# Performance work log

Hardware: AMD Instinct MI355X
Metric: run time of the kernel (lower is better)

## Reference

```python
import jax, jax.numpy as jnp
import numpy as np

B, C, F, G = 256, 4096, 64, 512   # batch, candidates, features, max taxi groups per sample
H1, H2 = 128, 128                 # scorer hidden dims
HB = 32                           # taxi bias net hidden dim
NEG = -1e9


def setup_inputs() -> dict:
    key = jax.random.key(0)
    ks = jax.random.split(key, 8)
    feats = jax.random.normal(ks[0], (B, C, F), jnp.float32)
    gids = jax.random.randint(ks[1], (B, C), -1, G)            # -1 = defer
    mask = (jax.random.uniform(ks[2], (B, C)) < 0.9).astype(jnp.float32)
    x_with_meta = jnp.concatenate(
        [feats, gids.astype(jnp.float32)[..., None], mask[..., None]], axis=-1)

    def lin(k, i, o):
        return (jax.random.normal(k, (i, o), jnp.float32) / np.sqrt(i)).astype(jnp.float32)

    return {
        "x_with_meta": x_with_meta,
        "W0": lin(ks[3], F, H1),  "b0": jnp.zeros((H1,), jnp.float32),
        "W1": lin(ks[4], H1, H2), "b1": jnp.zeros((H2,), jnp.float32),
        "W2": lin(ks[5], H2, 1),  "b2": jnp.zeros((1,), jnp.float32),
        "Wb0": lin(ks[6], 3, HB), "bb0": jnp.zeros((HB,), jnp.float32),
        "Wb1": lin(ks[7], HB, 1), "bb1": jnp.zeros((1,), jnp.float32),
    }


def _forward(x_with_meta, W0, b0, W1, b1, W2, b2, Wb0, bb0, Wb1, bb1):
    mask = x_with_meta[..., -1]                     # [B, C]
    gids = x_with_meta[..., -2].astype(jnp.int32)   # [B, C], -1 = defer
    feats = x_with_meta[..., :-2]                   # [B, C, F]

    # CandidateScorerMLP (dropout is identity at inference)
    h = jax.nn.relu(feats @ W0 + b0)
    h = jax.nn.relu(h @ W1 + b1)
    raw = (h @ W2 + b2)[..., 0]                     # [B, C]
    raw = jnp.where(mask > 0.0, raw, NEG)

    valid = (mask > 0.0) & (gids >= 0)              # [B, C]
    nseg = B * G + 1                                # +1 dummy segment for invalid/defer
    seg = jnp.where(valid, jnp.arange(B, dtype=jnp.int32)[:, None] * G + gids, B * G)
    segf = seg.reshape(-1)
    validf = valid.reshape(-1)
    rawf = raw.reshape(-1)

    cnt = jax.ops.segment_sum(validf.astype(jnp.float32), segf, num_segments=nseg)
    ssum = jax.ops.segment_sum(jnp.where(validf, rawf, 0.0), segf, num_segments=nseg)
    smax = jax.ops.segment_max(jnp.where(validf, rawf, NEG), segf, num_segments=nseg)
    smax = jnp.where(cnt > 0.0, smax, 0.0)          # sanitize empty segments
    mean = ssum / jnp.maximum(cnt, 1.0)
    multi = cnt > 1.0                               # normalization only for group size > 1

    # Per-group taxi quality bias from pooled stats [max, mean, size]
    stats = jnp.where(multi[:, None], jnp.stack([smax, mean, cnt], axis=-1), 0.0)  # [nseg, 3]
    bias = (jax.nn.relu(stats @ Wb0 + bb0) @ Wb1 + bb1)[:, 0]                      # [nseg]

    mean_c = mean[segf].reshape(B, C)
    max_c = smax[segf].reshape(B, C)
    bias_c = bias[segf].reshape(B, C)
    apply = valid & multi[segf].reshape(B, C)

    # raw - mean + max - 0.5*(max - raw) + bias  ==  1.5*raw - mean + 0.5*max + bias
    fair = jnp.where(apply, 1.5 * raw - mean_c + 0.5 * max_c + bias_c, raw)
    fair = jnp.where(mask > 0.0, fair, NEG)
    return fair, mask


def reference(x_with_meta, W0, b0, W1, b1, W2, b2, Wb0, bb0, Wb1, bb1):
    return _forward(x_with_meta, W0, b0, W1, b1, W2, b2, Wb0, bb0, Wb1, bb1)
```

## Files before the change

kernel.cpp:

```cpp
#include <hip/hip_runtime.h>
#include <hip/hip_bf16.h>

#define NB   256
#define NC   4096
#define NG   512
#define NH   128
#define NELEM (NB*NC)
#define LDX  66
#define NEGV (-1000000000.0f)
#define TILES 16

typedef __attribute__((ext_vector_type(8))) short short8;
typedef __attribute__((ext_vector_type(4))) float f32x4;

__device__ __forceinline__ unsigned pack2(float x, float y) {
    return (__float_as_uint(y) & 0xFFFF0000u) | (__float_as_uint(x) >> 16);
}
__device__ __forceinline__ unsigned short f2bf(float f) {
    unsigned u = __float_as_uint(f);
    return (unsigned short)((u + 0x7FFFu + ((u >> 16) & 1u)) >> 16);
}
__device__ __forceinline__ unsigned encf(float f) {
    unsigned u = __float_as_uint(f);
    return (u & 0x80000000u) ? ~u : (u | 0x80000000u);
}
__device__ __forceinline__ float decf(unsigned u) {
    unsigned v = (u & 0x80000000u) ? (u ^ 0x80000000u) : ~u;
    return __uint_as_float(v);
}
__device__ __forceinline__ f32x4 mfma_bf16(short8 a, short8 b, f32x4 c) {
    return __builtin_amdgcn_mfma_f32_16x16x32_bf16(a, b, c, 0, 0, 0);
}
__device__ __forceinline__ f32x4 mfma_fp8(long a, long b, f32x4 c) {
    return __builtin_amdgcn_mfma_f32_16x16x32_fp8_fp8(a, b, c, 0, 0, 0);
}

__device__ __forceinline__ void gload16(const float* g, float* lds) {
    __builtin_amdgcn_global_load_lds(
        (const __attribute__((address_space(1))) void*)g,
        (__attribute__((address_space(3))) void*)lds,
        16, 0, 0);
}

__global__ __launch_bounds__(512, 2) void k_fused(
        const float* __restrict__ X,
        const float* __restrict__ W0, const float* __restrict__ W1,
        const float* __restrict__ b0, const float* __restrict__ b1,
        const float* __restrict__ W2, const float* __restrict__ b2p,
        const float* __restrict__ Wb0, const float* __restrict__ bb0,
        const float* __restrict__ Wb1, const float* __restrict__ bb1,
        float* __restrict__ out) {
    __shared__ __align__(16) unsigned char sW1f[16384];
    __shared__ __align__(16) float sFeat[8][2048];
    __shared__ __align__(16) unsigned char sHs[8][4096];
    __shared__ float sB0[128];
    __shared__ float sB1W2[256];
    __shared__ __align__(16) float sraw[4096];
    __shared__ unsigned short smc[4096];
    __shared__ unsigned scnt[512];
    __shared__ float    ssum[512];
    __shared__ unsigned smx[512];
    __shared__ float    sdelta[512];
    __shared__ unsigned char smulti[512];

    const int t = threadIdx.x, w = t >> 6, l = t & 63;
    const int l15 = l & 15, g = l >> 4;
    const int rx = l15 & 7;
    const int b = blockIdx.x;

    float* fw = sFeat[w];
    unsigned char* hs = sHs[w];
    const size_t rowwave0 = (size_t)b * NC + w * 32;
    const int lrow0 = w * 32;

    const int r4 = l >> 4, sl = l & 15;
    const int offE = r4 * LDX + ((sl ^ r4) << 2);
    const int offO = r4 * LDX + ((sl ^ (r4 + 4)) << 2);

    {
        const float* gb = X + rowwave0 * LDX;
#pragma unroll
        for (int k = 0; k < 8; ++k)
            gload16(gb + k * 4 * LDX + ((k & 1) ? offO : offE), fw + k * 256);
    }
    float2 mt = make_float2(0.f, 0.f), mtN = make_float2(0.f, 0.f);
    if (l < 32) mt = *(const float2*)(X + (rowwave0 + l) * LDX + 64);

    unsigned short* sW0s = (unsigned short*)sraw;
    {
        const int j = t & 127, kq = t >> 7;
        unsigned pk[8];
#pragma unroll
        for (int kk = 0; kk < 16; kk += 2) {
            float v0 = W0[(kq * 16 + kk)     * NH + j];
            float v1 = W0[(kq * 16 + kk + 1) * NH + j];
            pk[kk >> 1] = (unsigned)f2bf(v0) | ((unsigned)f2bf(v1) << 16);
        }
        unsigned short* dst = sW0s + j * 64 + kq * 16;
        ((uint4*)dst)[0] = make_uint4(pk[0], pk[1], pk[2], pk[3]);
        ((uint4*)dst)[1] = make_uint4(pk[4], pk[5], pk[6], pk[7]);
    }
#pragma unroll
    for (int it = 0; it < 4; ++it) {
        const int j = t & 127, u = (t >> 7) + it * 4;
        float v[8];
#pragma unroll
        for (int d = 0; d < 8; ++d) v[d] = W1[(u * 8 + d) * NH + j];
        unsigned lo = (unsigned)__builtin_amdgcn_cvt_pk_fp8_f32(v[0], v[1], 0, false);
        lo = (unsigned)__builtin_amdgcn_cvt_pk_fp8_f32(v[2], v[3], (int)lo, true);
        unsigned hi = (unsigned)__builtin_amdgcn_cvt_pk_fp8_f32(v[4], v[5], 0, false);
        hi = (unsigned)__builtin_amdgcn_cvt_pk_fp8_f32(v[6], v[7], (int)hi, true);
        *(uint2*)(sW1f + (j * 16 + (u ^ (j & 7))) * 8) = make_uint2(lo, hi);
    }
    if (t < 128) { sB0[t] = b0[t]; sB1W2[t] = b1[t]; sB1W2[128 + t] = W2[t]; }
    scnt[t] = 0u; ssum[t] = 0.f; smx[t] = 0u;
    const float b2v = b2p[0];

    __syncthreads();

    short8 w0f[8][2];
#pragma unroll
    for (int n = 0; n < 8; ++n)
#pragma unroll
        for (int kk = 0; kk < 2; ++kk)
            w0f[n][kk] = *(const short8*)(sW0s + (n * 16 + l15) * 64 + kk * 32 + g * 8);

    __syncthreads();

    for (int tau = 0; tau < TILES; ++tau) {
        const size_t rowb = rowwave0 + (size_t)tau * 256;
        const int lrow = lrow0 + tau * 256;

        asm volatile("s_waitcnt vmcnt(0)" ::: "memory");
        __builtin_amdgcn_sched_barrier(0);

        short8 bfr[2][2];
#pragma unroll
        for (int rg = 0; rg < 2; ++rg)
#pragma unroll
            for (int kk = 0; kk < 2; ++kk) {
                const int row = rg * 16 + l15;
                const int u0 = kk * 8 + 2 * g;
                const float* base = fw + row * 64;
                float4 fa = *(const float4*)(base + ((u0 ^ rx) << 2));
                float4 fb = *(const float4*)(base + (((u0 + 1) ^ rx) << 2));
                union { unsigned u[4]; short8 s; } tu;
                tu.u[0] = pack2(fa.x, fa.y); tu.u[1] = pack2(fa.z, fa.w);
                tu.u[2] = pack2(fb.x, fb.y); tu.u[3] = pack2(fb.z, fb.w);
                bfr[rg][kk] = tu.s;
            }

        asm volatile("s_waitcnt lgkmcnt(0)" ::: "memory");
        __builtin_amdgcn_sched_barrier(0);
        if (tau + 1 < TILES) {
            const float* gb = X + (rowb + 256) * LDX;
#pragma unroll
            for (int k = 0; k < 8; ++k)
                gload16(gb + k * 4 * LDX + ((k & 1) ? offO : offE), fw + k * 256);
            if (l < 32) mtN = *(const float2*)(X + (rowb + 256 + l) * LDX + 64);
        }
        __builtin_amdgcn_sched_barrier(0);

#pragma unroll
        for (int nh = 0; nh < 2; ++nh) {
            f32x4 acc[4][2];
#pragma unroll
            for (int n4 = 0; n4 < 4; ++n4)
#pragma unroll
                for (int rg = 0; rg < 2; ++rg) acc[n4][rg] = (f32x4){0.f, 0.f, 0.f, 0.f};
#pragma unroll
            for (int n4 = 0; n4 < 4; ++n4) {
                const int n = nh * 4 + n4;
#pragma unroll
                for (int rg = 0; rg < 2; ++rg) {
                    acc[n4][rg] = mfma_bf16(w0f[n][0], bfr[rg][0], acc[n4][rg]);
                    acc[n4][rg] = mfma_bf16(w0f[n][1], bfr[rg][1], acc[n4][rg]);
                }
            }
#pragma unroll
            for (int n4 = 0; n4 < 4; ++n4) {
                const int n = nh * 4 + n4;
                const int c0 = n * 16 + g * 4;
                const float bv0 = sB0[c0], bv1 = sB0[c0+1], bv2 = sB0[c0+2], bv3 = sB0[c0+3];
                const int u = (2 * n + (g >> 1)) ^ rx;
#pragma unroll
                for (int rg = 0; rg < 2; ++rg) {
                    unsigned d0 = (unsigned)__builtin_amdgcn_cvt_pk_fp8_f32(
                        fmaxf(acc[n4][rg][0] + bv0, 0.f), fmaxf(acc[n4][rg][1] + bv1, 0.f), 0, false);
                    d0 = (unsigned)__builtin_amdgcn_cvt_pk_fp8_f32(
                        fmaxf(acc[n4][rg][2] + bv2, 0.f), fmaxf(acc[n4][rg][3] + bv3, 0.f), (int)d0, true);
                    *(unsigned*)(hs + ((rg * 16 + l15) * 16 + u) * 8 + (g & 1) * 4) = d0;
                }
            }
        }

        asm volatile("" ::: "memory");

        long a2[2][4];
#pragma unroll
        for (int rg = 0; rg < 2; ++rg)
#pragma unroll
            for (int kk = 0; kk < 4; ++kk)
                a2[rg][kk] = *(const long*)(hs + ((rg * 16 + l15) * 16 + ((kk * 4 + g) ^ rx)) * 8);

        float rq[2][4] = {{0.f,0.f,0.f,0.f},{0.f,0.f,0.f,0.f}};
#pragma unroll
        for (int n = 0; n < 8; ++n) {
            f32x4 acc2[2] = {(f32x4){0.f,0.f,0.f,0.f}, (f32x4){0.f,0.f,0.f,0.f}};
            const unsigned char* wrow = sW1f + (n * 16 + l15) * 128;
#pragma unroll
            for (int kk = 0; kk < 4; ++kk) {
                long bb = *(const long*)(wrow + ((kk * 4 + g) ^ rx) * 8);
                acc2[0] = mfma_fp8(a2[0][kk], bb, acc2[0]);
                acc2[1] = mfma_fp8(a2[1][kk], bb, acc2[1]);
            }
            const float b1v = sB1W2[n * 16 + l15], w2v = sB1W2[128 + n * 16 + l15];
#pragma unroll
            for (int rg = 0; rg < 2; ++rg)
#pragma unroll
                for (int q = 0; q < 4; ++q)
                    rq[rg][q] += fmaxf(acc2[rg][q] + b1v, 0.f) * w2v;
        }

#pragma unroll
        for (int off = 1; off < 16; off <<= 1)
#pragma unroll
            for (int rg = 0; rg < 2; ++rg)
#pragma unroll
                for (int q = 0; q < 4; ++q)
                    rq[rg][q] += __shfl_xor(rq[rg][q], off, 64);
        if (l15 == 0) {
#pragma unroll
            for (int rg = 0; rg < 2; ++rg) {
                const int lm0 = lrow + rg * 16 + g * 4;
                *(float4*)(sraw + lm0) = make_float4(rq[rg][0] + b2v, rq[rg][1] + b2v,
                                                     rq[rg][2] + b2v, rq[rg][3] + b2v);
            }
        }
        if (l < 32) {
            const unsigned pmcu = ((unsigned)((int)mt.x + 1) << 1) | (mt.y > 0.f ? 1u : 0u);
            smc[lrow + l] = (unsigned short)pmcu;
        }
        mt = mtN;
    }

    __syncthreads();

#pragma unroll
    for (int it = 0; it < 8; ++it) {
        int m = it * 512 + t;
        unsigned c = smc[m];
        if ((c & 1u) && (c >> 1)) {
            int s = (int)(c >> 1) - 1;
            float r = sraw[m];
            atomicAdd(&scnt[s], 1u);
            atomicAdd(&ssum[s], r);
            atomicMax(&smx[s], encf(r));
        }
    }
    __syncthreads();

    {
        unsigned c = scnt[t];
        float delta = 0.f; unsigned char multi = 0;
        if (c > 1) {
            float smaxv = decf(smx[t]);
            float mean = ssum[t] / (float)c;
            float bias = bb1[0];
#pragma unroll
            for (int j = 0; j < 32; ++j) {
                float h = smaxv * Wb0[j] + mean * Wb0[32 + j] + (float)c * Wb0[64 + j] + bb0[j];
                bias += fmaxf(h, 0.f) * Wb1[j];
            }
            delta = 0.5f * smaxv - mean + bias;
            multi = 1;
        }
        sdelta[t] = delta; smulti[t] = multi;
    }
    __syncthreads();

    const size_t gbase = (size_t)b * NC;
#pragma unroll
    for (int it = 0; it < 2; ++it) {
        int i = it * 512 + t;
        int m0 = i * 4;
        float4 rv = *(const float4*)(sraw + m0);
        const float r[4] = {rv.x, rv.y, rv.z, rv.w};
        float fair[4], msk[4];
#pragma unroll
        for (int j = 0; j < 4; ++j) {
            unsigned c = smc[m0 + j];
            msk[j] = (c & 1u) ? 1.0f : 0.0f;
            float f;
            if (c & 1u) {
                f = r[j];
                if (c >> 1) {
                    int s = (int)(c >> 1) - 1;
                    if (smulti[s]) f = 1.5f * r[j] + sdelta[s];
                }
            } else {
                f = NEGV;
            }
            fair[j] = f;
        }
        *(float4*)(out + gbase + m0) = make_float4(fair[0], fair[1], fair[2], fair[3]);
        *(float4*)(out + NELEM + gbase + m0) = make_float4(msk[0], msk[1], msk[2], msk[3]);
    }
}

extern "C" void kernel_launch(void* const* d_in, const int* in_sizes, int n_in,
                              void* d_out, int out_size, void* d_ws, size_t ws_size,
                              hipStream_t stream) {
    const float* X   = (const float*)d_in[0];
    const float* W0  = (const float*)d_in[1];
    const float* b0  = (const float*)d_in[2];
    const float* W1  = (const float*)d_in[3];
    const float* b1  = (const float*)d_in[4];
    const float* W2  = (const float*)d_in[5];
    const float* b2  = (const float*)d_in[6];
    const float* Wb0 = (const float*)d_in[7];
    const float* bb0 = (const float*)d_in[8];
    const float* Wb1 = (const float*)d_in[9];
    const float* bb1 = (const float*)d_in[10];

    k_fused<<<NB, 512, 0, stream>>>(X, W0, W1, b0, b1, W2, b2,
                                    Wb0, bb0, Wb1, bb1, (float*)d_out);
}
```

Measured before the change: 76.02 us.

## Split per-tile feature staging into two halves with partial vmcnt waits

The first-layer MFMA stage of each 32-row tile is split into two 16-row halves. Each half waits only for its own async global-to-LDS loads (vmcnt(5) instead of vmcnt(0)), and the next tile's prefetch is issued in two matching halves, so the wait on memory for the second half can overlap with compute on the first. This relies on exact counts of outstanding vector memory ops and on the scalar meta load being ordered last; a miscount would make the code read stale LDS data.

```diff
diff --git a/kernel.cpp b/kernel.cpp
--- a/kernel.cpp
+++ b/kernel.cpp
@@ -85,6 +85,7 @@
     }
     float2 mt = make_float2(0.f, 0.f), mtN = make_float2(0.f, 0.f);
     if (l < 32) mt = *(const float2*)(X + (rowwave0 + l) * LDX + 64);
+    __builtin_amdgcn_sched_barrier(0);
 
     unsigned short* sW0s = (unsigned short*)sraw;
     {
@@ -131,51 +132,41 @@
         const size_t rowb = rowwave0 + (size_t)tau * 256;
         const int lrow = lrow0 + tau * 256;
 
-        asm volatile("s_waitcnt vmcnt(0)" ::: "memory");
-        __builtin_amdgcn_sched_barrier(0);
-
-        short8 bfr[2][2];
-#pragma unroll
-        for (int rg = 0; rg < 2; ++rg)
-#pragma unroll
-            for (int kk = 0; kk < 2; ++kk) {
-                const int row = rg * 16 + l15;
-                const int u0 = kk * 8 + 2 * g;
-                const float* base = fw + row * 64;
-                float4 fa = *(const float4*)(base + ((u0 ^ rx) << 2));
-                float4 fb = *(const float4*)(base + (((u0 + 1) ^ rx) << 2));
-                union { unsigned u[4]; short8 s; } tu;
-                tu.u[0] = pack2(fa.x, fa.y); tu.u[1] = pack2(fa.z, fa.w);
-                tu.u[2] = pack2(fb.x, fb.y); tu.u[3] = pack2(fb.z, fb.w);
-                bfr[rg][kk] = tu.s;
-            }
-
+        asm volatile("s_waitcnt vmcnt(5)" ::: "memory");
+        __builtin_amdgcn_sched_barrier(0);
+
+        short8 bfrA[2];
+#pragma unroll
+        for (int kk = 0; kk < 2; ++kk) {
+            const int u0 = kk * 8 + 2 * g;
+            const float* base = fw + l15 * 64;
+            float4 fa = *(const float4*)(base + ((u0 ^ rx) << 2));
+            float4 fb = *(const float4*)(base + (((u0 + 1) ^ rx) << 2));
+            union { unsigned u[4]; short8 s; } tu;
+            tu.u[0] = pack2(fa.x, fa.y); tu.u[1] = pack2(fa.z, fa.w);
+            tu.u[2] = pack2(fb.x, fb.y); tu.u[3] = pack2(fb.z, fb.w);
+            bfrA[kk] = tu.s;
+        }
         asm volatile("s_waitcnt lgkmcnt(0)" ::: "memory");
         __builtin_amdgcn_sched_barrier(0);
         if (tau + 1 < TILES) {
             const float* gb = X + (rowb + 256) * LDX;
 #pragma unroll
-            for (int k = 0; k < 8; ++k)
+            for (int k = 0; k < 4; ++k)
                 gload16(gb + k * 4 * LDX + ((k & 1) ? offO : offE), fw + k * 256);
-            if (l < 32) mtN = *(const float2*)(X + (rowb + 256 + l) * LDX + 64);
         }
         __builtin_amdgcn_sched_barrier(0);
 
 #pragma unroll
         for (int nh = 0; nh < 2; ++nh) {
-            f32x4 acc[4][2];
-#pragma unroll
-            for (int n4 = 0; n4 < 4; ++n4)
-#pragma unroll
-                for (int rg = 0; rg < 2; ++rg) acc[n4][rg] = (f32x4){0.f, 0.f, 0.f, 0.f};
+            f32x4 acc[4];
+#pragma unroll
+            for (int n4 = 0; n4 < 4; ++n4) acc[n4] = (f32x4){0.f, 0.f, 0.f, 0.f};
 #pragma unroll
             for (int n4 = 0; n4 < 4; ++n4) {
                 const int n = nh * 4 + n4;
-#pragma unroll
-                for (int rg = 0; rg < 2; ++rg) {
-                    acc[n4][rg] = mfma_bf16(w0f[n][0], bfr[rg][0], acc[n4][rg]);
-                    acc[n4][rg] = mfma_bf16(w0f[n][1], bfr[rg][1], acc[n4][rg]);
-                }
+                acc[n4] = mfma_bf16(w0f[n][0], bfrA[0], acc[n4]);
+                acc[n4] = mfma_bf16(w0f[n][1], bfrA[1], acc[n4]);
             }
 #pragma unroll
             for (int n4 = 0; n4 < 4; ++n4) {
@@ -183,14 +174,63 @@
                 const int c0 = n * 16 + g * 4;
                 const float bv0 = sB0[c0], bv1 = sB0[c0+1], bv2 = sB0[c0+2], bv3 = sB0[c0+3];
                 const int u = (2 * n + (g >> 1)) ^ rx;
-#pragma unroll
-                for (int rg = 0; rg < 2; ++rg) {
-                    unsigned d0 = (unsigned)__builtin_amdgcn_cvt_pk_fp8_f32(
-                        fmaxf(acc[n4][rg][0] + bv0, 0.f), fmaxf(acc[n4][rg][1] + bv1, 0.f), 0, false);
-                    d0 = (unsigned)__builtin_amdgcn_cvt_pk_fp8_f32(
-                        fmaxf(acc[n4][rg][2] + bv2, 0.f), fmaxf(acc[n4][rg][3] + bv3, 0.f), (int)d0, true);
-                    *(unsigned*)(hs + ((rg * 16 + l15) * 16 + u) * 8 + (g & 1) * 4) = d0;
-                }
+                unsigned d0 = (unsigned)__builtin_amdgcn_cvt_pk_fp8_f32(
+                    fmaxf(acc[n4][0] + bv0, 0.f), fmaxf(acc[n4][1] + bv1, 0.f), 0, false);
+                d0 = (unsigned)__builtin_amdgcn_cvt_pk_fp8_f32(
+                    fmaxf(acc[n4][2] + bv2, 0.f), fmaxf(acc[n4][3] + bv3, 0.f), (int)d0, true);
+                *(unsigned*)(hs + (l15 * 16 + u) * 8 + (g & 1) * 4) = d0;
+            }
+        }
+
+        if (tau + 1 < TILES) asm volatile("s_waitcnt vmcnt(5)" ::: "memory");
+        else                 asm volatile("s_waitcnt vmcnt(1)" ::: "memory");
+        __builtin_amdgcn_sched_barrier(0);
+
+        short8 bfrB[2];
+#pragma unroll
+        for (int kk = 0; kk < 2; ++kk) {
+            const int u0 = kk * 8 + 2 * g;
+            const float* base = fw + (16 + l15) * 64;
+            float4 fa = *(const float4*)(base + ((u0 ^ rx) << 2));
+            float4 fb = *(const float4*)(base + (((u0 + 1) ^ rx) << 2));
+            union { unsigned u[4]; short8 s; } tu;
+            tu.u[0] = pack2(fa.x, fa.y); tu.u[1] = pack2(fa.z, fa.w);
+            tu.u[2] = pack2(fb.x, fb.y); tu.u[3] = pack2(fb.z, fb.w);
+            bfrB[kk] = tu.s;
+        }
+        asm volatile("s_waitcnt lgkmcnt(0)" ::: "memory");
+        __builtin_amdgcn_sched_barrier(0);
+        if (tau + 1 < TILES) {
+            const float* gb = X + (rowb + 256) * LDX;
+#pragma unroll
+            for (int k = 4; k < 8; ++k)
+                gload16(gb + k * 4 * LDX + ((k & 1) ? offO : offE), fw + k * 256);
+            if (l < 32) mtN = *(const float2*)(X + (rowb + 256 + l) * LDX + 64);
+        }
+        __builtin_amdgcn_sched_barrier(0);
+
+#pragma unroll
+        for (int nh = 0; nh < 2; ++nh) {
+            f32x4 acc[4];
+#pragma unroll
+            for (int n4 = 0; n4 < 4; ++n4) acc[n4] = (f32x4){0.f, 0.f, 0.f, 0.f};
+#pragma unroll
+            for (int n4 = 0; n4 < 4; ++n4) {
+                const int n = nh * 4 + n4;
+                acc[n4] = mfma_bf16(w0f[n][0], bfrB[0], acc[n4]);
+                acc[n4] = mfma_bf16(w0f[n][1], bfrB[1], acc[n4]);
+            }
+#pragma unroll
+            for (int n4 = 0; n4 < 4; ++n4) {
+                const int n = nh * 4 + n4;
+                const int c0 = n * 16 + g * 4;
+                const float bv0 = sB0[c0], bv1 = sB0[c0+1], bv2 = sB0[c0+2], bv3 = sB0[c0+3];
+                const int u = (2 * n + (g >> 1)) ^ rx;
+                unsigned d0 = (unsigned)__builtin_amdgcn_cvt_pk_fp8_f32(
+                    fmaxf(acc[n4][0] + bv0, 0.f), fmaxf(acc[n4][1] + bv1, 0.f), 0, false);
+                d0 = (unsigned)__builtin_amdgcn_cvt_pk_fp8_f32(
+                    fmaxf(acc[n4][2] + bv2, 0.f), fmaxf(acc[n4][3] + bv3, 0.f), (int)d0, true);
+                *(unsigned*)(hs + ((16 + l15) * 16 + u) * 8 + (g & 1) * 4) = d0;
             }
         }
 
```

New measurement: 82.56 us. 1.09x slower.
